# Kernel optimization log

Measured on AMD Instinct MI355X. Metric: run time of the kernel, lower is better.

Reference implementation:

```python
import jax, jax.numpy as jnp
import numpy as np

D_MODEL = 768
N_HEADS = 12
N_KV = 4
D_HEAD = 64
WINDOW = 512
GLOBAL = 64
THETA = 10000.0


def setup_inputs() -> dict:
    key = jax.random.key(0)
    ks = jax.random.split(key, 5)
    B, T = 2, 2048
    s = D_MODEL ** -0.5
    return {
        "x": jax.random.normal(ks[0], (B, T, D_MODEL), jnp.float32),
        "wq": jax.random.normal(ks[1], (D_MODEL, N_HEADS * D_HEAD), jnp.float32) * s,
        "wk": jax.random.normal(ks[2], (D_MODEL, N_KV * D_HEAD), jnp.float32) * s,
        "wv": jax.random.normal(ks[3], (D_MODEL, N_KV * D_HEAD), jnp.float32) * s,
        "wo": jax.random.normal(ks[4], (N_HEADS * D_HEAD, D_MODEL), jnp.float32) * s,
    }


def _rotate_half(x):
    h = x.shape[-1] // 2
    return jnp.concatenate([-x[..., h:], x[..., :h]], axis=-1)


def _rope_tables(T, dtype):
    inv_freq = 1.0 / (THETA ** (jnp.arange(0, D_HEAD, 2, dtype=jnp.float32) / D_HEAD))
    freqs = jnp.outer(jnp.arange(T, dtype=jnp.float32), inv_freq)  # [T, D_HEAD/2]
    emb = jnp.concatenate([freqs, freqs], axis=-1)  # [T, D_HEAD]
    return jnp.cos(emb).astype(dtype), jnp.sin(emb).astype(dtype)


def reference(x, wq, wk, wv, wo):
    B, T, _ = x.shape
    # projections -> [B, H, T, D]
    q = (x @ wq).reshape(B, T, N_HEADS, D_HEAD).transpose(0, 2, 1, 3)
    k = (x @ wk).reshape(B, T, N_KV, D_HEAD).transpose(0, 2, 1, 3)
    v = (x @ wv).reshape(B, T, N_KV, D_HEAD).transpose(0, 2, 1, 3)
    # RoPE (broadcast [T,D] over batch/heads)
    cos, sin = _rope_tables(T, x.dtype)
    q = q * cos + _rotate_half(q) * sin
    k = k * cos + _rotate_half(k) * sin
    new_k, new_v = k, v  # kv cache before GQA expansion
    # GQA expansion: each kv head repeated kv_groups consecutive times
    groups = N_HEADS // N_KV
    k = jnp.repeat(k, groups, axis=1)
    v = jnp.repeat(v, groups, axis=1)
    scale = jnp.asarray(D_HEAD, x.dtype) ** 0.5
    scores = jnp.einsum("bhqd,bhkd->bhqk", q, k) / scale
    # sliding-window causal + global-token mask (Longformer-style)
    i = jnp.arange(T)[:, None]
    j = jnp.arange(T)[None, :]
    allowed = (j <= i) & ((j > i - WINDOW) | (j < GLOBAL) | (i < GLOBAL))
    scores = jnp.where(allowed, scores, -jnp.inf)
    weights = jax.nn.softmax(scores, axis=-1)
    out = jnp.einsum("bhqk,bhkd->bhqd", weights, v)
    out = out.transpose(0, 2, 1, 3).reshape(B, T, N_HEADS * D_HEAD)
    return out @ wo, (new_k, new_v)
```

## Files before the change

### kernel.cpp

```cpp
#include <hip/hip_runtime.h>
#include <hip/hip_bf16.h>

#define BATCH 2
#define SEQ 2048
#define DMODEL 768
#define NHEADS 12
#define NKV 4
#define DHEAD 64
#define WIN 512
#define GLB 64
#define ROWS (BATCH * SEQ)

typedef short short8 __attribute__((ext_vector_type(8)));
typedef float f32x4 __attribute__((ext_vector_type(4)));

__device__ inline short f2bs(float f) {
    unsigned u = __float_as_uint(f);
    return (short)((u + 0x7fffu + ((u >> 16) & 1u)) >> 16);
}

__device__ inline void cp16(const short* g, short* l) {
    __builtin_amdgcn_global_load_lds(
        (const __attribute__((address_space(1))) unsigned int*)g,
        (__attribute__((address_space(3))) unsigned int*)l, 16, 0, 0);
}

__global__ __launch_bounds__(256) void transp_all(
    const float* __restrict__ wq, const float* __restrict__ wk,
    const float* __restrict__ wv, const float* __restrict__ wo,
    short* __restrict__ wqkvT, short* __restrict__ woT) {
    __shared__ float t[32][33];
    int bid = blockIdx.x;
    const float* src; short* dst; int N;
    if (bid < 576)      { src = wq; dst = wqkvT; N = DMODEL; }
    else if (bid < 768) { src = wk; dst = wqkvT + DMODEL * DMODEL; N = 256; bid -= 576; }
    else if (bid < 960) { src = wv; dst = wqkvT + (DMODEL + 256) * DMODEL; N = 256; bid -= 768; }
    else                { src = wo; dst = woT; N = DMODEL; bid -= 960; }
    const int ntx = N >> 5;
    const int k0 = (bid / ntx) << 5, n0 = (bid % ntx) << 5;
    const int x = threadIdx.x & 31, y = threadIdx.x >> 5;
#pragma unroll
    for (int i = 0; i < 32; i += 8)
        t[y + i][x] = src[(long)(k0 + y + i) * N + n0 + x];
    __syncthreads();
#pragma unroll
    for (int i = 0; i < 32; i += 8)
        dst[(long)(n0 + y + i) * DMODEL + k0 + x] = f2bs(t[x][y + i]);
}

__global__ __launch_bounds__(256) void prep_kv(const float* __restrict__ Vin,
                                               short* __restrict__ Vout,
                                               float* Kc, short* __restrict__ Kb) {
    __shared__ float t[32][33];
    const int bid = blockIdx.x;
    if (bid < 2048) {
        const int tid = bid * 256 + threadIdx.x;
        const int j = tid & 31;
        const int kvh = (tid >> 5) & 3;
        const int row = tid >> 7;
        const int trow = row & (SEQ - 1), b = row >> 11;
        const float inv = expf(-(float)j * 0.2878231366f);
        float s, c;
        sincosf((float)trow * inv, &s, &c);
        const long off = ((long)(b * NKV + kvh) * SEQ + trow) << 6;
        float* p = Kc + off;
        const float x1 = p[j], x2 = p[j + 32];
        const float y1 = x1 * c - x2 * s, y2 = x2 * c + x1 * s;
        p[j] = y1;
        p[j + 32] = y2;
        Kb[off + j] = f2bs(y1);
        Kb[off + j + 32] = f2bs(y2);
    } else {
        const int b2 = bid - 2048;
        const int tx = b2 & 63, dy = (b2 >> 6) & 1;
        const long bkv = b2 >> 7;
        const float* ip = Vin + bkv * SEQ * DHEAD;
        short* op = Vout + bkv * DHEAD * SEQ;
        const int t0 = tx * 32, d0 = dy * 32;
        const int x = threadIdx.x & 31, y = threadIdx.x >> 5;
#pragma unroll
        for (int i = 0; i < 32; i += 8)
            t[y + i][x] = ip[(long)(t0 + y + i) * DHEAD + d0 + x];
        __syncthreads();
        const int pan = t0 >> 6, tin = t0 & 63;
#pragma unroll
        for (int i = 0; i < 32; i += 8)
            op[(long)pan * 4096 + (d0 + y + i) * 64 + tin + x] = f2bs(t[x][y + i]);
    }
}

#define LST 40

template <typename TA, int MODE>
__global__ __launch_bounds__(256) void gemm_tn(const TA* __restrict__ A,
                                               const short* __restrict__ Bt,
                                               float* __restrict__ Cq,
                                               float* __restrict__ Ck,
                                               float* __restrict__ Cv,
                                               int M, int N, int K) {
    __shared__ short As_[128 * LST];
    __shared__ short Bs_[128 * LST];
    const int tid = threadIdx.x;
    const int lane = tid & 63, w = tid >> 6;
    const int m_ = lane & 15, quad = lane >> 4;
    const int wm = w >> 1, wn = w & 1;
    const long bm = (long)blockIdx.y * 128, bn = (long)blockIdx.x * 128;
    const int sr = tid >> 1, sh = (tid & 1) * 16;

    f32x4 acc[4][4];
#pragma unroll
    for (int i = 0; i < 4; ++i)
#pragma unroll
        for (int j = 0; j < 4; ++j) acc[i][j] = (f32x4){0.f, 0.f, 0.f, 0.f};

    for (int k0 = 0; k0 < K; k0 += 32) {
        short av[16], bv[16];
        if (sizeof(TA) == 4) {
            const float* ap = (const float*)A + (bm + sr) * K + k0 + sh;
            float ff[16];
#pragma unroll
            for (int i = 0; i < 4; ++i) *(float4*)&ff[4 * i] = ((const float4*)ap)[i];
#pragma unroll
            for (int i = 0; i < 16; ++i) av[i] = f2bs(ff[i]);
        } else {
            const short* ap = (const short*)A + (bm + sr) * K + k0 + sh;
            *(uint4*)&av[0] = ((const uint4*)ap)[0];
            *(uint4*)&av[8] = ((const uint4*)ap)[1];
        }
        {
            const short* bp = Bt + (bn + sr) * K + k0 + sh;
            *(uint4*)&bv[0] = ((const uint4*)bp)[0];
            *(uint4*)&bv[8] = ((const uint4*)bp)[1];
        }
        __syncthreads();
        short* ad = &As_[sr * LST + sh];
        short* bd = &Bs_[sr * LST + sh];
#pragma unroll
        for (int i = 0; i < 4; ++i) {
            ((uint2*)ad)[i] = ((uint2*)av)[i];
            ((uint2*)bd)[i] = ((uint2*)bv)[i];
        }
        __syncthreads();

        short8 af[4], bf[4];
#pragma unroll
        for (int i = 0; i < 4; ++i)
            af[i] = *(const short8*)&As_[(wm * 64 + i * 16 + m_) * LST + quad * 8];
#pragma unroll
        for (int j = 0; j < 4; ++j)
            bf[j] = *(const short8*)&Bs_[(wn * 64 + j * 16 + m_) * LST + quad * 8];
#pragma unroll
        for (int i = 0; i < 4; ++i)
#pragma unroll
            for (int j = 0; j < 4; ++j)
                acc[i][j] = __builtin_amdgcn_mfma_f32_16x16x32_bf16(af[i], bf[j], acc[i][j], 0, 0, 0);
    }

#pragma unroll
    for (int i = 0; i < 4; ++i) {
        const int row0 = (int)bm + wm * 64 + i * 16 + quad * 4;
#pragma unroll
        for (int j = 0; j < 4; ++j) {
            const int col = (int)bn + wn * 64 + j * 16 + m_;
#pragma unroll
            for (int r = 0; r < 4; ++r) {
                const int rw = row0 + r;
                const float val = acc[i][j][r];
                if (MODE == 1) {
                    if (col < DMODEL) {
                        Cq[(long)rw * DMODEL + col] = val;
                    } else {
                        const int c2 = col - DMODEL;
                        const int hh = (c2 >> 6) & 3, d = c2 & 63;
                        long oidx = (((long)((rw >> 11) * NKV + hh) * SEQ + (rw & (SEQ - 1))) << 6) | d;
                        ((c2 >> 8) ? Cv : Ck)[oidx] = val;
                    }
                } else {
                    Cq[(long)rw * N + col] = val;
                }
            }
        }
    }
}

__global__ __launch_bounds__(384) void flash6(
    const float* __restrict__ Qf, const short* __restrict__ Kb,
    const short* __restrict__ Vt, short* __restrict__ ATT) {
    __shared__ short Kbuf[2][64 * 64];
    __shared__ short Vbuf[2][64 * 64];
    __shared__ short Pl[6][16 * 64];
    const int tid = threadIdx.x;
    const int w = tid >> 6, lane = tid & 63;
    const int m_ = lane & 15, quad = lane >> 4;
    const int sw = m_ & 7;
    const int bkv = blockIdx.x >> 6;
    const int t0 = (63 - (blockIdx.x & 63)) << 5;
    const int b = bkv >> 2, kvh = bkv & 3;
    const int h = kvh * 3 + (w >> 1);
    const int qg = w & 1;
    const int trw = t0 + (qg << 4);
    const int tq = trw + m_;
    const long kgb = ((long)bkv * SEQ) << 6;
    const long vgb = (long)bkv * SEQ * DHEAD;

    const int soff = ((lane >> 3) << 6) + (((lane & 7) ^ (lane >> 3)) << 3);

    short8 qf0, qf1;
    {
        const float* qpf = Qf + (long)(b * SEQ + tq) * DMODEL + h * DHEAD + quad * 8;
        float xx[8], yy[8];
        *(float4*)&xx[0] = ((const float4*)qpf)[0];
        *(float4*)&xx[4] = ((const float4*)qpf)[1];
        *(float4*)&yy[0] = ((const float4*)(qpf + 32))[0];
        *(float4*)&yy[4] = ((const float4*)(qpf + 32))[1];
#pragma unroll
        for (int jj = 0; jj < 8; ++jj) {
            const int j = quad * 8 + jj;
            const float inv = expf(-(float)j * 0.2878231366f);
            float s_, c_;
            sincosf((float)tq * inv, &s_, &c_);
            qf0[jj] = f2bs((xx[jj] * c_ - yy[jj] * s_) * 0.125f);
            qf1[jj] = f2bs((yy[jj] * c_ + xx[jj] * s_) * 0.125f);
        }
    }

    f32x4 of[4];
#pragma unroll
    for (int i = 0; i < 4; ++i) of[i] = (f32x4){0.f, 0.f, 0.f, 0.f};
    float mr = -1e30f, lr = 0.f;

    int wlo = t0 - (WIN - 1);
    if (wlo < GLB) wlo = GLB;
    wlo &= ~63;
    const int nwin = (t0 + 31 >= wlo) ? (((t0 + 31 - wlo) >> 6) + 1) : 0;
    const int ntile = 1 + nwin;
    auto kb_of = [&](int j) { return (j == 0) ? 0 : (wlo + ((j - 1) << 6)); };

    auto stage = [&](int kb, int bs) {
#pragma unroll
        for (int r = 0; r < 3; ++r) {
            const int ch = w + 6 * r;
            if (ch < 8) {
                cp16(Kb + kgb + ((long)(kb + (ch << 3)) << 6) + soff,
                     &Kbuf[bs][ch << 9]);
            } else if (ch < 16) {
                const int cv = ch - 8;
                cp16(Vt + vgb + (((long)kb >> 6) << 12) + (cv << 9) + soff,
                     &Vbuf[bs][cv << 9]);
            }
        }
    };

    stage(kb_of(0), 0);
    asm volatile("s_waitcnt vmcnt(0)" ::: "memory");
    asm volatile("s_barrier" ::: "memory");

    for (int tI = 0; tI < ntile; ++tI) {
        const int kb = kb_of(tI);
        const int bs = tI & 1;
        if (tI + 1 < ntile) stage(kb_of(tI + 1), bs ^ 1);

        short8 kf[8], vf[8];
#pragma unroll
        for (int st = 0; st < 4; ++st)
#pragma unroll
            for (int hh = 0; hh < 2; ++hh)
                kf[st * 2 + hh] = *(const short8*)&Kbuf[bs][(st * 16 + m_) * 64 + (((hh * 4 + quad) ^ sw) << 3)];
#pragma unroll
        for (int dt = 0; dt < 4; ++dt)
#pragma unroll
            for (int kh = 0; kh < 2; ++kh)
                vf[dt * 2 + kh] = *(const short8*)&Vbuf[bs][(dt * 16 + m_) * 64 + (((kh * 4 + quad) ^ sw) << 3)];

        f32x4 s[4];
        __builtin_amdgcn_s_setprio(1);
#pragma unroll
        for (int st = 0; st < 4; ++st) {
            f32x4 a = (f32x4){0.f, 0.f, 0.f, 0.f};
            a = __builtin_amdgcn_mfma_f32_16x16x32_bf16(kf[st * 2 + 0], qf0, a, 0, 0, 0);
            a = __builtin_amdgcn_mfma_f32_16x16x32_bf16(kf[st * 2 + 1], qf1, a, 0, 0, 0);
            s[st] = a;
        }
        __builtin_amdgcn_s_setprio(0);

        const bool fully = (kb + 63 <= trw) &&
                           ((kb >= trw + 16 - WIN) || (kb + 63 < GLB) || (trw + 15 < GLB));
        if (!fully) {
#pragma unroll
            for (int st = 0; st < 4; ++st) {
#pragma unroll
                for (int r = 0; r < 4; ++r) {
                    const int key = kb + st * 16 + quad * 4 + r;
                    const bool ok = (key <= tq) && ((key > tq - WIN) || (key < GLB) || (tq < GLB));
                    if (!ok) s[st][r] = -1e30f;
                }
            }
        }

        float tm = -1e30f;
#pragma unroll
        for (int st = 0; st < 4; ++st)
#pragma unroll
            for (int r = 0; r < 4; ++r) tm = fmaxf(tm, s[st][r]);
        tm = fmaxf(tm, __shfl_xor(tm, 16, 64));
        tm = fmaxf(tm, __shfl_xor(tm, 32, 64));
        if (!__all(tm <= mr)) {
            const float mnew = fmaxf(mr, tm);
            const float alpha = __expf(mr - mnew);
            mr = mnew;
            lr *= alpha;
#pragma unroll
            for (int dt = 0; dt < 4; ++dt)
#pragma unroll
                for (int r = 0; r < 4; ++r) of[dt][r] *= alpha;
        }
        float rs = 0.f;
#pragma unroll
        for (int st = 0; st < 4; ++st) {
            float p0 = __expf(s[st][0] - mr);
            float p1 = __expf(s[st][1] - mr);
            float p2 = __expf(s[st][2] - mr);
            float p3 = __expf(s[st][3] - mr);
            rs += (p0 + p1) + (p2 + p3);
            union { short sh[4]; unsigned long long u; } pk;
            pk.sh[0] = f2bs(p0); pk.sh[1] = f2bs(p1);
            pk.sh[2] = f2bs(p2); pk.sh[3] = f2bs(p3);
            *(unsigned long long*)&Pl[w][m_ * 64 + (((st * 2 + (quad >> 1)) ^ sw) << 3) + ((quad & 1) << 2)] = pk.u;
        }
        rs += __shfl_xor(rs, 16, 64);
        rs += __shfl_xor(rs, 32, 64);
        lr += rs;

        short8 pf[2];
#pragma unroll
        for (int kh = 0; kh < 2; ++kh)
            pf[kh] = *(const short8*)&Pl[w][m_ * 64 + (((kh * 4 + quad) ^ sw) << 3)];

        __builtin_amdgcn_s_setprio(1);
#pragma unroll
        for (int dt = 0; dt < 4; ++dt) {
            of[dt] = __builtin_amdgcn_mfma_f32_16x16x32_bf16(vf[dt * 2 + 0], pf[0], of[dt], 0, 0, 0);
            of[dt] = __builtin_amdgcn_mfma_f32_16x16x32_bf16(vf[dt * 2 + 1], pf[1], of[dt], 0, 0, 0);
        }
        __builtin_amdgcn_s_setprio(0);

        if (tI + 1 < ntile) {
            asm volatile("s_waitcnt vmcnt(0)" ::: "memory");
            asm volatile("s_barrier" ::: "memory");
        }
    }

    const float inv = 1.0f / lr;
    short* op = ATT + (long)(b * SEQ + tq) * DMODEL + h * DHEAD + quad * 4;
#pragma unroll
    for (int dt = 0; dt < 4; ++dt) {
        union { short sh[4]; unsigned long long u; } pk;
#pragma unroll
        for (int r = 0; r < 4; ++r) pk.sh[r] = f2bs(of[dt][r] * inv);
        *(unsigned long long*)(op + dt * 16) = pk.u;
    }
}

extern "C" void kernel_launch(void* const* d_in, const int* in_sizes, int n_in,
                              void* d_out, int out_size, void* d_ws, size_t ws_size,
                              hipStream_t stream) {
    const float* x = (const float*)d_in[0];
    const float* wq = (const float*)d_in[1];
    const float* wk = (const float*)d_in[2];
    const float* wv = (const float*)d_in[3];
    const float* wo = (const float*)d_in[4];
    float* out = (float*)d_out;
    float* out_k = out + (long)ROWS * DMODEL;
    float* out_v = out_k + (long)BATCH * NKV * SEQ * DHEAD;

    short* regA = (short*)d_ws;
    short* wqkvT = regA;
    short* ATTb = regA;
    short* woT = regA + (long)ROWS * DMODEL;
    short* KbB = woT + (long)DMODEL * DMODEL;
    short* VtB = KbB + (long)BATCH * NKV * SEQ * DHEAD;

    transp_all<<<1536, 256, 0, stream>>>(wq, wk, wv, wo, wqkvT, woT);
    gemm_tn<float, 1><<<dim3((DMODEL + 2 * NKV * DHEAD) / 128, ROWS / 128), 256, 0, stream>>>(
        x, wqkvT, out, out_k, out_v, ROWS, DMODEL + 2 * NKV * DHEAD, DMODEL);
    prep_kv<<<2048 + 1024, 256, 0, stream>>>(out_v, VtB, out_k, KbB);
    flash6<<<BATCH * NKV * (SEQ / 32), 384, 0, stream>>>(out, KbB, VtB, ATTb);
    gemm_tn<short, 0><<<dim3(DMODEL / 128, ROWS / 128), 256, 0, stream>>>(
        ATTb, woT, out, nullptr, nullptr, ROWS, DMODEL, DMODEL);
}
```

Measured before the change: 161.2 us.

## Pre-convert x to bf16 and double-buffer GEMM tiles via direct global-to-LDS loads

The fp32-to-bf16 conversion of x moves out of the QKV GEMM into extra blocks of the weight-transpose kernel, so both GEMMs read bf16 A operands. The GEMM mainloop is rewritten to use global_load_lds into XOR-swizzled, double-buffered 128x64 LDS tiles, prefetching the next K-step while MFMAs run, with setprio around the MFMA block. This targets load latency and LDS bank conflicts. It costs an extra round trip of x through workspace memory and doubles the LDS footprint, which may lower occupancy.

Result: faster. 138.3 us (-14.2%).

```diff
diff --git a/kernel.cpp b/kernel.cpp
--- a/kernel.cpp
+++ b/kernel.cpp
@@ -28,9 +28,21 @@
 __global__ __launch_bounds__(256) void transp_all(
     const float* __restrict__ wq, const float* __restrict__ wk,
     const float* __restrict__ wv, const float* __restrict__ wo,
-    short* __restrict__ wqkvT, short* __restrict__ woT) {
+    short* __restrict__ wqkvT, short* __restrict__ woT,
+    const float* __restrict__ x, short* __restrict__ xb) {
     __shared__ float t[32][33];
     int bid = blockIdx.x;
+    if (bid >= 1536) {
+        const long i = ((long)(bid - 1536) * 256 + threadIdx.x) * 8;
+        float ff[8];
+        *(float4*)&ff[0] = ((const float4*)(x + i))[0];
+        *(float4*)&ff[4] = ((const float4*)(x + i))[1];
+        short8 o;
+#pragma unroll
+        for (int j = 0; j < 8; ++j) o[j] = f2bs(ff[j]);
+        *(short8*)(xb + i) = o;
+        return;
+    }
     const float* src; short* dst; int N;
     if (bid < 576)      { src = wq; dst = wqkvT; N = DMODEL; }
     else if (bid < 768) { src = wk; dst = wqkvT + DMODEL * DMODEL; N = 256; bid -= 576; }
@@ -38,14 +50,14 @@
     else                { src = wo; dst = woT; N = DMODEL; bid -= 960; }
     const int ntx = N >> 5;
     const int k0 = (bid / ntx) << 5, n0 = (bid % ntx) << 5;
-    const int x = threadIdx.x & 31, y = threadIdx.x >> 5;
+    const int x_ = threadIdx.x & 31, y = threadIdx.x >> 5;
 #pragma unroll
     for (int i = 0; i < 32; i += 8)
-        t[y + i][x] = src[(long)(k0 + y + i) * N + n0 + x];
+        t[y + i][x_] = src[(long)(k0 + y + i) * N + n0 + x_];
     __syncthreads();
 #pragma unroll
     for (int i = 0; i < 32; i += 8)
-        dst[(long)(n0 + y + i) * DMODEL + k0 + x] = f2bs(t[x][y + i]);
+        dst[(long)(n0 + y + i) * DMODEL + k0 + x_] = f2bs(t[x_][y + i]);
 }
 
 __global__ __launch_bounds__(256) void prep_kv(const float* __restrict__ Vin,
@@ -89,23 +101,22 @@
     }
 }
 
-#define LST 40
-
-template <typename TA, int MODE>
-__global__ __launch_bounds__(256) void gemm_tn(const TA* __restrict__ A,
+template <int MODE>
+__global__ __launch_bounds__(256) void gemm_tn(const short* __restrict__ A,
                                                const short* __restrict__ Bt,
                                                float* __restrict__ Cq,
                                                float* __restrict__ Ck,
                                                float* __restrict__ Cv,
                                                int M, int N, int K) {
-    __shared__ short As_[128 * LST];
-    __shared__ short Bs_[128 * LST];
+    __shared__ short As_[2][128 * 64];
+    __shared__ short Bs_[2][128 * 64];
     const int tid = threadIdx.x;
     const int lane = tid & 63, w = tid >> 6;
     const int m_ = lane & 15, quad = lane >> 4;
+    const int sw = m_ & 7;
     const int wm = w >> 1, wn = w & 1;
     const long bm = (long)blockIdx.y * 128, bn = (long)blockIdx.x * 128;
-    const int sr = tid >> 1, sh = (tid & 1) * 16;
+    const int soff = (lane >> 3) * K + (((lane & 7) ^ (lane >> 3)) << 3);
 
     f32x4 acc[4][4];
 #pragma unroll
@@ -113,47 +124,47 @@
 #pragma unroll
         for (int j = 0; j < 4; ++j) acc[i][j] = (f32x4){0.f, 0.f, 0.f, 0.f};
 
-    for (int k0 = 0; k0 < K; k0 += 32) {
-        short av[16], bv[16];
-        if (sizeof(TA) == 4) {
-            const float* ap = (const float*)A + (bm + sr) * K + k0 + sh;
-            float ff[16];
-#pragma unroll
-            for (int i = 0; i < 4; ++i) *(float4*)&ff[4 * i] = ((const float4*)ap)[i];
-#pragma unroll
-            for (int i = 0; i < 16; ++i) av[i] = f2bs(ff[i]);
-        } else {
-            const short* ap = (const short*)A + (bm + sr) * K + k0 + sh;
-            *(uint4*)&av[0] = ((const uint4*)ap)[0];
-            *(uint4*)&av[8] = ((const uint4*)ap)[1];
-        }
-        {
-            const short* bp = Bt + (bn + sr) * K + k0 + sh;
-            *(uint4*)&bv[0] = ((const uint4*)bp)[0];
-            *(uint4*)&bv[8] = ((const uint4*)bp)[1];
-        }
-        __syncthreads();
-        short* ad = &As_[sr * LST + sh];
-        short* bd = &Bs_[sr * LST + sh];
-#pragma unroll
-        for (int i = 0; i < 4; ++i) {
-            ((uint2*)ad)[i] = ((uint2*)av)[i];
-            ((uint2*)bd)[i] = ((uint2*)bv)[i];
-        }
-        __syncthreads();
-
-        short8 af[4], bf[4];
-#pragma unroll
-        for (int i = 0; i < 4; ++i)
-            af[i] = *(const short8*)&As_[(wm * 64 + i * 16 + m_) * LST + quad * 8];
-#pragma unroll
-        for (int j = 0; j < 4; ++j)
-            bf[j] = *(const short8*)&Bs_[(wn * 64 + j * 16 + m_) * LST + quad * 8];
-#pragma unroll
-        for (int i = 0; i < 4; ++i)
+    auto stage = [&](int k0, int bs) {
+#pragma unroll
+        for (int r = 0; r < 8; ++r) {
+            const int ch = (w << 3) + r;
+            if (ch < 16)
+                cp16(A + (bm + (ch << 3)) * K + k0 + soff, &As_[bs][ch << 9]);
+            else
+                cp16(Bt + (bn + ((ch - 16) << 3)) * K + k0 + soff,
+                     &Bs_[bs][(ch - 16) << 9]);
+        }
+    };
+
+    stage(0, 0);
+    asm volatile("s_waitcnt vmcnt(0)" ::: "memory");
+    asm volatile("s_barrier" ::: "memory");
+
+    const int nk = K >> 6;
+    for (int ks = 0; ks < nk; ++ks) {
+        const int bs = ks & 1;
+        if (ks + 1 < nk) stage((ks + 1) << 6, bs ^ 1);
+#pragma unroll
+        for (int kh = 0; kh < 2; ++kh) {
+            short8 af[4], bf[4];
+#pragma unroll
+            for (int i = 0; i < 4; ++i)
+                af[i] = *(const short8*)&As_[bs][(wm * 64 + i * 16 + m_) * 64 + (((kh * 4 + quad) ^ sw) << 3)];
 #pragma unroll
             for (int j = 0; j < 4; ++j)
-                acc[i][j] = __builtin_amdgcn_mfma_f32_16x16x32_bf16(af[i], bf[j], acc[i][j], 0, 0, 0);
+                bf[j] = *(const short8*)&Bs_[bs][(wn * 64 + j * 16 + m_) * 64 + (((kh * 4 + quad) ^ sw) << 3)];
+            __builtin_amdgcn_s_setprio(1);
+#pragma unroll
+            for (int i = 0; i < 4; ++i)
+#pragma unroll
+                for (int j = 0; j < 4; ++j)
+                    acc[i][j] = __builtin_amdgcn_mfma_f32_16x16x32_bf16(af[i], bf[j], acc[i][j], 0, 0, 0);
+            __builtin_amdgcn_s_setprio(0);
+        }
+        if (ks + 1 < nk) {
+            asm volatile("s_waitcnt vmcnt(0)" ::: "memory");
+            asm volatile("s_barrier" ::: "memory");
+        }
     }
 
 #pragma unroll
@@ -379,12 +390,13 @@
     short* woT = regA + (long)ROWS * DMODEL;
     short* KbB = woT + (long)DMODEL * DMODEL;
     short* VtB = KbB + (long)BATCH * NKV * SEQ * DHEAD;
-
-    transp_all<<<1536, 256, 0, stream>>>(wq, wk, wv, wo, wqkvT, woT);
-    gemm_tn<float, 1><<<dim3((DMODEL + 2 * NKV * DHEAD) / 128, ROWS / 128), 256, 0, stream>>>(
-        x, wqkvT, out, out_k, out_v, ROWS, DMODEL + 2 * NKV * DHEAD, DMODEL);
+    short* xb = VtB + (long)BATCH * NKV * SEQ * DHEAD;
+
+    transp_all<<<3072, 256, 0, stream>>>(wq, wk, wv, wo, wqkvT, woT, x, xb);
+    gemm_tn<1><<<dim3((DMODEL + 2 * NKV * DHEAD) / 128, ROWS / 128), 256, 0, stream>>>(
+        xb, wqkvT, out, out_k, out_v, ROWS, DMODEL + 2 * NKV * DHEAD, DMODEL);
     prep_kv<<<2048 + 1024, 256, 0, stream>>>(out_v, VtB, out_k, KbB);
     flash6<<<BATCH * NKV * (SEQ / 32), 384, 0, stream>>>(out, KbB, VtB, ATTb);
-    gemm_tn<short, 0><<<dim3(DMODEL / 128, ROWS / 128), 256, 0, stream>>>(
+    gemm_tn<0><<<dim3(DMODEL / 128, ROWS / 128), 256, 0, stream>>>(
         ATTb, woT, out, nullptr, nullptr, ROWS, DMODEL, DMODEL);
 }
```
